# Performance work log

Hardware: AMD Instinct MI355X
Metric: run time of the kernel (lower is better)

Reference implementation:

```python
import jax, jax.numpy as jnp
import numpy as np

SELF_DIM = 6
GS_DIM = 100

def _lin(x, w, b):
    return x @ w + b

def setup_inputs() -> dict:
    key = jax.random.key(0)
    ks = jax.random.split(key, 24)
    def p(k, shape, fan_in):
        return jax.random.normal(k, shape, dtype=jnp.float32) * (1.0 / np.sqrt(fan_in))
    state = jax.random.normal(ks[0], (16384, 20, 13), dtype=jnp.float32)
    inp = {"state": state}
    # mlp1: 13 -> 150 -> 100 -> 100
    inp["w1"], inp["b1"] = p(ks[1], (13, 150), 13), jnp.zeros((150,), jnp.float32)
    inp["w2"], inp["b2"] = p(ks[2], (150, 100), 150), jnp.zeros((100,), jnp.float32)
    inp["w3"], inp["b3"] = p(ks[3], (100, 100), 100), jnp.zeros((100,), jnp.float32)
    # attention: 200 -> 100 -> 100 -> 1
    inp["a1"], inp["ab1"] = p(ks[4], (200, 100), 200), jnp.zeros((100,), jnp.float32)
    inp["a2"], inp["ab2"] = p(ks[5], (100, 100), 100), jnp.zeros((100,), jnp.float32)
    inp["a3"], inp["ab3"] = p(ks[6], (100, 1), 100), jnp.zeros((1,), jnp.float32)
    # mlp2: 106 -> 150 -> 100 -> 100 -> 1
    inp["m1"], inp["mb1"] = p(ks[7], (106, 150), 106), jnp.zeros((150,), jnp.float32)
    inp["m2"], inp["mb2"] = p(ks[8], (150, 100), 150), jnp.zeros((100,), jnp.float32)
    inp["m3"], inp["mb3"] = p(ks[9], (100, 100), 100), jnp.zeros((100,), jnp.float32)
    inp["m4"], inp["mb4"] = p(ks[10], (100, 1), 100), jnp.zeros((1,), jnp.float32)
    return inp

def reference(state, w1, b1, w2, b2, w3, b3, a1, ab1, a2, ab2, a3, ab3,
              m1, mb1, m2, mb2, m3, mb3, m4, mb4):
    B, N, D = state.shape
    self_state = state[:, 0, :SELF_DIM]                      # [B, 6]
    x = state.reshape(B * N, D)
    h = jax.nn.relu(_lin(x, w1, b1))
    h = jax.nn.relu(_lin(h, w2, b2))
    mlp1_out = _lin(h, w3, b3)                               # [B*N, 100]
    feat = mlp1_out.reshape(B, N, GS_DIM)
    global_state = jnp.broadcast_to(feat.mean(axis=1, keepdims=True), (B, N, GS_DIM))
    att_in = jnp.concatenate([feat, global_state], axis=-1)  # [B, N, 200]
    s = jax.nn.relu(_lin(att_in, a1, ab1))
    s = jax.nn.relu(_lin(s, a2, ab2))
    scores = jax.nn.relu(_lin(s, a3, ab3))[..., 0]           # [B, N]
    weights = jax.nn.softmax(scores, axis=1)                 # [B, N]
    weighted_feature = jnp.einsum('bn,bnd->bd', weights, feat)
    joint = jnp.concatenate([self_state, weighted_feature], axis=-1)  # [B, 106]
    v = jax.nn.relu(_lin(joint, m1, mb1))
    v = jax.nn.relu(_lin(v, m2, mb2))
    v = jax.nn.relu(_lin(v, m3, mb3))
    value = _lin(v, m4, mb4)                                 # [B, 1]
    return value
```

## Files before the change

### kernel.cpp

```cpp
#include <hip/hip_runtime.h>
#include <math.h>

#define NTHR 512
#define NB 4
#define NROWSR (NB * 20)

typedef _Float16 h8v __attribute__((ext_vector_type(8)));
typedef _Float16 h2v __attribute__((ext_vector_type(2)));
using f4 = __attribute__((ext_vector_type(4))) float;

__device__ __forceinline__ h2v cvt_pk_h2(float a, float b) {
  return __builtin_bit_cast(h2v, __builtin_amdgcn_cvt_pkrtz(a, b));
}

#define H1_OFF 0
#define H1_PK 168
#define H2_OFF 26880
#define H2_PK 136
#define FEAT_OFF 0
#define FEAT_PK 136
#define S1_OFF 26880
#define S1_PK 136
#define XS_OFF 26880
#define XS_PK 40
#define GS_OFF S1_OFF
#define POOL1 48640

#define L1B 0
#define L2B 20
#define L3B 90
#define A1B 146
#define A2B 202
#define M1B 258
#define M2B 338
#define M3B 408
#define A1GB 464
#define BIAS_BYTE 532480
#define JOINT_BYTE 536576

#define BO_B1 0
#define BO_B2 160
#define BO_B3 320
#define BO_AB1 480
#define BO_MB1 800
#define BO_MB2 960
#define BO_MB3 1120

#define K2ROWS 64
#define K2THR 256
#define K2_JT_OFF 0
#define K2_V1_OFF 17408
#define K2_POOL 38912

__device__ __forceinline__ float relu_f(float v) { return fmaxf(v, 0.f); }
__device__ __forceinline__ float h2f(ushort u) {
  return (float)__builtin_bit_cast(_Float16, u);
}
__device__ __forceinline__ ushort f2h(float v) {
  return __builtin_bit_cast(ushort, (_Float16)v);
}
__device__ __forceinline__ uint pk2h(float a, float b) {
  return (uint)f2h(a) | ((uint)f2h(b) << 16);
}

__device__ __forceinline__ float4 load4_guard(const float* __restrict__ a, int of4, int C) {
  float4 v;
  if (of4 + 3 < C) v = *(const float4*)(a + of4);
  else {
    v.x = (of4 + 0 < C) ? a[of4 + 0] : 0.f;
    v.y = (of4 + 1 < C) ? a[of4 + 1] : 0.f;
    v.z = (of4 + 2 < C) ? a[of4 + 2] : 0.f;
    v.w = (of4 + 3 < C) ? a[of4 + 3] : 0.f;
  }
  return v;
}

__global__ __launch_bounds__(64) void prep_kernel(
    const float* __restrict__ w1, const float* __restrict__ w2,
    const float* __restrict__ w3, const float* __restrict__ a1,
    const float* __restrict__ a2, const float* __restrict__ m1,
    const float* __restrict__ m2, const float* __restrict__ m3,
    const float* __restrict__ b1, const float* __restrict__ b2,
    const float* __restrict__ b3, const float* __restrict__ ab1,
    const float* __restrict__ mb1, const float* __restrict__ mb2,
    const float* __restrict__ mb3,
    uint4* __restrict__ ws) {
  const int job = blockIdx.x;
  const int lane = threadIdx.x;
  if (job == 260) {
    ushort* bh = (ushort*)((char*)ws + BIAS_BYTE);
    for (int idx = lane; idx < 1280; idx += 64) {
      const int reg = idx / 160, off = idx - reg * 160;
      const float* src = nullptr; int C = 0;
      switch (reg) {
        case 0: src = b1;  C = 150; break;
        case 1: src = b2;  C = 100; break;
        case 2: src = b3;  C = 100; break;
        case 3: src = ab1; C = 100; break;
        case 4: src = nullptr; C = 0; break;
        case 5: src = mb1; C = 150; break;
        case 6: src = mb2; C = 100; break;
        default: src = mb3; C = 100; break;
      }
      bh[idx] = (off < C) ? f2h(src[off]) : (ushort)0;
    }
    return;
  }
  const float* W;
  int K, C, NT, base, kb, nt, i;
  if (job < 10)       { W = w1; K = 13;  C = 150; NT = 10; base = L1B; kb = 0; nt = job; }
  else if (job < 45)  { W = w2; K = 150; C = 100; NT = 7;  base = L2B; i = job - 10;  kb = i / 7;  nt = i % 7; }
  else if (job < 73)  { W = w3; K = 100; C = 100; NT = 7;  base = L3B; i = job - 45;  kb = i / 7;  nt = i % 7; }
  else if (job < 101) { W = a1; K = 100; C = 100; NT = 7;  base = A1B; i = job - 73;  kb = i / 7;  nt = i % 7; }
  else if (job < 129) { W = a2; K = 100; C = 100; NT = 7;  base = A2B; i = job - 101; kb = i / 7;  nt = i % 7; }
  else if (job < 169) { W = m1; K = 106; C = 150; NT = 10; base = M1B; i = job - 129; kb = i / 10; nt = i % 10; }
  else if (job < 204) { W = m2; K = 150; C = 100; NT = 7;  base = M2B; i = job - 169; kb = i / 7;  nt = i % 7; }
  else if (job < 232) { W = m3; K = 100; C = 100; NT = 7;  base = M3B; i = job - 204; kb = i / 7;  nt = i % 7; }
  else                { W = a1 + 10000; K = 100; C = 100; NT = 7; base = A1GB; i = job - 232; kb = i / 7; nt = i % 7; }
  const int r = lane & 15, g = lane >> 4;
  const int j = nt * 16 + r;
  uint hi[8], lo[8];
  for (int e = 0; e < 8; ++e) {
    int k = kb * 32 + g * 8 + e;
    float v = (k < K && j < C) ? W[k * C + j] : 0.f;
    _Float16 hh = (_Float16)v;
    float hf = (float)hh;
    _Float16 ll = (_Float16)(v - hf);
    hi[e] = (uint)__builtin_bit_cast(ushort, hh);
    lo[e] = (uint)__builtin_bit_cast(ushort, ll);
  }
  uint4 vh = { hi[0] | (hi[1] << 16), hi[2] | (hi[3] << 16),
               hi[4] | (hi[5] << 16), hi[6] | (hi[7] << 16) };
  uint4 vl = { lo[0] | (lo[1] << 16), lo[2] | (lo[3] << 16),
               lo[4] | (lo[5] << 16), lo[6] | (lo[7] << 16) };
  ws[(size_t)(base + (kb * NT + nt) * 2 + 0) * 64 + lane] = vh;
  ws[(size_t)(base + (kb * NT + nt) * 2 + 1) * 64 + lane] = vl;
}

template <int KB, int NT, int C, int MODE, int ROWS, bool W8, int TERMS>
__device__ __forceinline__ void mfma_layer(
    char* pool, int inOff, int PKin, int outOff, int PKout,
    const h8v* __restrict__ wsB, const ushort* __restrict__ biasH,
    const float* __restrict__ biasF, const ushort* gpartH, float* sceL,
    const float* __restrict__ a3, int lane, int wid) {
  constexpr int MTL = ROWS / 16;
  const int r = lane & 15, g = lane >> 4;
  const char* Ain = pool + inOff;
  int wlo, mtb, mte;
  if constexpr (W8) {
    wlo = wid & 3;
    const int whi = wid >> 2;
    mtb = whi ? 3 : 0; mte = whi ? MTL : 3;
  } else { wlo = wid; mtb = 0; mte = MTL; }
  for (int nt = wlo; nt < NT; nt += 4) {
    h8v wh[KB], wl[KB];
#pragma unroll
    for (int kb = 0; kb < KB; ++kb) {
      wh[kb] = wsB[((kb * NT + nt) * 2 + 0) * 64 + lane];
      if constexpr (TERMS == 2)
        wl[kb] = wsB[((kb * NT + nt) * 2 + 1) * 64 + lane];
    }
    const int of = nt * 16 + g * 4;
    uint2 bp;
    float4 b4, a34;
    if constexpr (MODE == 3) {
      b4 = load4_guard(biasF, of, C);
      a34 = load4_guard(a3, of, C);
    } else {
      bp = *(const uint2*)(biasH + of);
    }
    for (int mt = mtb; mt < mte; ++mt) {
      const int ar = mt * 16 + r;
      f4 acc = {0.f, 0.f, 0.f, 0.f};
      const char* aP = Ain + ar * (PKin * 2) + g * 16;
#pragma unroll
      for (int kb = 0; kb < KB; ++kb) {
        h8v a = *(const h8v*)(aP + kb * 64);
        acc = __builtin_amdgcn_mfma_f32_16x16x32_f16(wh[kb], a, acc, 0, 0, 0);
        if constexpr (TERMS == 2)
          acc = __builtin_amdgcn_mfma_f32_16x16x32_f16(wl[kb], a, acc, 0, 0, 0);
      }
      if constexpr (MODE == 3) {
        float v0 = fmaxf(acc[0] + b4.x, 0.f), v1 = fmaxf(acc[1] + b4.y, 0.f);
        float v2 = fmaxf(acc[2] + b4.z, 0.f), v3 = fmaxf(acc[3] + b4.w, 0.f);
        float val = v0 * a34.x + v1 * a34.y + v2 * a34.z + v3 * a34.w;
        val += __shfl_xor(val, 16);
        val += __shfl_xor(val, 32);
        if (lane < 16) atomicAdd(&sceL[ar], val);
      } else {
        h2v lo = cvt_pk_h2(acc[0], acc[1]);
        h2v hi = cvt_pk_h2(acc[2], acc[3]);
        lo += __builtin_bit_cast(h2v, bp.x);
        hi += __builtin_bit_cast(h2v, bp.y);
        if constexpr (MODE == 2) {
          uint2 gp = *(const uint2*)(gpartH + (ar / 20) * 112 + of);
          lo += __builtin_bit_cast(h2v, gp.x);
          hi += __builtin_bit_cast(h2v, gp.y);
        }
        if constexpr (MODE != 1) {
          h2v z = {(_Float16)0.f, (_Float16)0.f};
          lo = __builtin_elementwise_max(lo, z);
          hi = __builtin_elementwise_max(hi, z);
        }
        *(uint2*)((ushort*)(pool + outOff) + ar * PKout + of) =
            uint2{__builtin_bit_cast(uint, lo), __builtin_bit_cast(uint, hi)};
      }
    }
  }
}

template <int ROWSZ, int PK>
__device__ __forceinline__ void zero_tail(char* pool, int off, int tid) {
  if (tid < ROWSZ) {
    uint4* z = (uint4*)((ushort*)(pool + off) + (size_t)tid * PK + 112);
    z[0] = uint4{0, 0, 0, 0};
    z[1] = uint4{0, 0, 0, 0};
  }
}

__global__ __launch_bounds__(NTHR, 6) void value_net_kernel(
    const float* __restrict__ state,
    const float* __restrict__ ab2,
    const float* __restrict__ a3, const float* __restrict__ ab3,
    const uint4* __restrict__ ws, ushort* __restrict__ jointgH) {
  __shared__ char pool[POOL1];
  __shared__ ushort gpartH[NB * 112];
  __shared__ float sceL[NROWSR], swL[NROWSR];

  const int tid = threadIdx.x;
  const int lane = tid & 63, wid = tid >> 6;
  const int b0 = blockIdx.x * NB;
  const h8v* wsb = (const h8v*)ws;
  const ushort* biasH = (const ushort*)((const char*)ws + BIAS_BYTE);

  for (int i = tid; i < NROWSR * XS_PK; i += NTHR) {
    int row = i / XS_PK, k = i - row * XS_PK;
    float v = (k < 13) ? state[((size_t)b0 * 20 + row) * 13 + k] : 0.f;
    ((ushort*)(pool + XS_OFF))[row * XS_PK + k] = f2h(v);
  }
  if (tid < NROWSR) sceL[tid] = 0.f;
  __syncthreads();

  mfma_layer<1, 10, 150, 0, NROWSR, true, 1>(
      pool, XS_OFF, XS_PK, H1_OFF, H1_PK, wsb + L1B * 64, biasH + BO_B1,
      nullptr, nullptr, nullptr, nullptr, lane, wid);
  __syncthreads();

  zero_tail<NROWSR, H2_PK>(pool, H2_OFF, tid);
  mfma_layer<5, 7, 100, 0, NROWSR, true, 1>(
      pool, H1_OFF, H1_PK, H2_OFF, H2_PK, wsb + L2B * 64, biasH + BO_B2,
      nullptr, nullptr, nullptr, nullptr, lane, wid);
  __syncthreads();

  zero_tail<NROWSR, FEAT_PK>(pool, FEAT_OFF, tid);
  mfma_layer<4, 7, 100, 1, NROWSR, true, 1>(
      pool, H2_OFF, H2_PK, FEAT_OFF, FEAT_PK, wsb + L3B * 64, biasH + BO_B3,
      nullptr, nullptr, nullptr, nullptr, lane, wid);
  __syncthreads();

  if (tid < NB * 100) {
    const int b = tid / 100, d = tid - b * 100;
    const ushort* f = (const ushort*)(pool + FEAT_OFF);
    float s = 0.f;
    for (int n = 0; n < 20; ++n) s += h2f(f[(b * 20 + n) * FEAT_PK + d]);
    ((ushort*)(pool + GS_OFF))[b * 136 + d] = f2h(s * 0.05f);
  } else if (tid < NB * 100 + NB * 28) {
    const int idx = tid - NB * 100;
    ((ushort*)(pool + GS_OFF))[(idx / 28) * 136 + 100 + (idx % 28)] = 0;
  }
  __syncthreads();

  if (wid < 7) {
    const int r = lane & 15, g = lane >> 4;
    const int nt = wid;
    const h8v* wsg = wsb + A1GB * 64;
    h8v wh[4];
#pragma unroll
    for (int kb = 0; kb < 4; ++kb)
      wh[kb] = wsg[((kb * 7 + nt) * 2 + 0) * 64 + lane];
    const char* aP = pool + GS_OFF + (r & 3) * (136 * 2) + g * 16;
    f4 acc = {0.f, 0.f, 0.f, 0.f};
#pragma unroll
    for (int kb = 0; kb < 4; ++kb) {
      h8v a = *(const h8v*)(aP + kb * 64);
      acc = __builtin_amdgcn_mfma_f32_16x16x32_f16(wh[kb], a, acc, 0, 0, 0);
    }
    const int of = nt * 16 + g * 4;
    if (r < 4) {
      uint2 pk = { pk2h(acc[0], acc[1]), pk2h(acc[2], acc[3]) };
      *(uint2*)(gpartH + r * 112 + of) = pk;
    }
  }
  __syncthreads();

  mfma_layer<4, 7, 100, 2, NROWSR, true, 1>(
      pool, FEAT_OFF, FEAT_PK, S1_OFF, S1_PK, wsb + A1B * 64, biasH + BO_AB1,
      nullptr, gpartH, nullptr, nullptr, lane, wid);
  __syncthreads();

  mfma_layer<4, 7, 100, 3, NROWSR, true, 1>(
      pool, S1_OFF, S1_PK, 0, 0, wsb + A2B * 64, nullptr,
      ab2, nullptr, sceL, a3, lane, wid);
  __syncthreads();

  if (tid < 128) {
    const int b = tid >> 5, l = tid & 31;
    const float ab3v = ab3[0];
    float s = (l < 20) ? relu_f(sceL[b * 20 + l] + ab3v) : -1e30f;
    float m = s;
#pragma unroll
    for (int d = 1; d < 32; d <<= 1) m = fmaxf(m, __shfl_xor(m, d));
    float e = (l < 20) ? __expf(s - m) : 0.f;
    float sum = e;
#pragma unroll
    for (int d = 1; d < 32; d <<= 1) sum += __shfl_xor(sum, d);
    if (l < 20) swL[b * 20 + l] = e / sum;
  }
  __syncthreads();

  for (int it = tid; it < NB * 200; it += NTHR) {
    const int b = it / 200, rem = it - b * 200;
    const int d = rem >> 1, half = rem & 1;
    const ushort* f = (const ushort*)(pool + FEAT_OFF);
    float acc = 0.f;
    for (int n = half * 10; n < half * 10 + 10; ++n)
      acc += swL[b * 20 + n] * h2f(f[(b * 20 + n) * FEAT_PK + d]);
    acc += __shfl_xor(acc, 1);
    if (half == 0) jointgH[(size_t)(b0 + b) * 106 + 6 + d] = f2h(acc);
  }
  if (tid < NB * 6) {
    const int b = tid / 6, i = tid - b * 6;
    jointgH[(size_t)(b0 + b) * 106 + i] = f2h(state[((size_t)(b0 + b)) * 260 + i]);
  }
}

__global__ __launch_bounds__(K2THR) void mlp2_kernel(
    const ushort* __restrict__ jointgH,
    const float* __restrict__ m4, const float* __restrict__ mb4,
    const uint4* __restrict__ ws, float* __restrict__ out) {
  __shared__ char pool[K2_POOL];
  __shared__ float m4L[100];
  const int tid = threadIdx.x, lane = tid & 63, wid = tid >> 6;
  const size_t r0 = (size_t)blockIdx.x * K2ROWS;
  const h8v* wsb = (const h8v*)ws;
  const ushort* biasH = (const ushort*)((const char*)ws + BIAS_BYTE);

  for (int i = tid; i < K2ROWS * 136; i += K2THR) {
    int row = i / 136, k = i - row * 136;
    ((ushort*)(pool + K2_JT_OFF))[row * 136 + k] =
        (k < 106) ? jointgH[(r0 + row) * 106 + k] : (ushort)0;
  }
  if (tid < 100) m4L[tid] = m4[tid];
  __syncthreads();

  mfma_layer<4, 10, 150, 0, K2ROWS, false, 2>(
      pool, K2_JT_OFF, 136, K2_V1_OFF, 168, wsb + M1B * 64, biasH + BO_MB1,
      nullptr, nullptr, nullptr, nullptr, lane, wid);
  __syncthreads();

  zero_tail<K2ROWS, 136>(pool, 0, tid);
  mfma_layer<5, 7, 100, 0, K2ROWS, false, 2>(
      pool, K2_V1_OFF, 168, 0, 136, wsb + M2B * 64, biasH + BO_MB2,
      nullptr, nullptr, nullptr, nullptr, lane, wid);
  __syncthreads();

  mfma_layer<4, 7, 100, 0, K2ROWS, false, 2>(
      pool, 0, 136, K2_V1_OFF, 136, wsb + M3B * 64, biasH + BO_MB3,
      nullptr, nullptr, nullptr, nullptr, lane, wid);
  __syncthreads();

  {
    const int row = tid >> 2, seg = tid & 3;
    const ushort* v3 = (const ushort*)(pool + K2_V1_OFF);
    float s = 0.f;
    for (int k = seg; k < 100; k += 4) s += h2f(v3[row * 136 + k]) * m4L[k];
    s += __shfl_xor(s, 1);
    s += __shfl_xor(s, 2);
    if (seg == 0) out[r0 + row] = s + mb4[0];
  }
}

extern "C" void kernel_launch(void* const* d_in, const int* in_sizes, int n_in,
                              void* d_out, int out_size, void* d_ws, size_t ws_size,
                              hipStream_t stream) {
  const float* state = (const float*)d_in[0];
  const float* w1 = (const float*)d_in[1];
  const float* b1 = (const float*)d_in[2];
  const float* w2 = (const float*)d_in[3];
  const float* b2 = (const float*)d_in[4];
  const float* w3 = (const float*)d_in[5];
  const float* b3 = (const float*)d_in[6];
  const float* a1 = (const float*)d_in[7];
  const float* ab1 = (const float*)d_in[8];
  const float* a2 = (const float*)d_in[9];
  const float* ab2 = (const float*)d_in[10];
  const float* a3 = (const float*)d_in[11];
  const float* ab3 = (const float*)d_in[12];
  const float* m1 = (const float*)d_in[13];
  const float* mb1 = (const float*)d_in[14];
  const float* m2 = (const float*)d_in[15];
  const float* mb2 = (const float*)d_in[16];
  const float* m3 = (const float*)d_in[17];
  const float* mb3 = (const float*)d_in[18];
  const float* m4 = (const float*)d_in[19];
  const float* mb4 = (const float*)d_in[20];
  float* out = (float*)d_out;
  uint4* ws = (uint4*)d_ws;
  ushort* jointgH = (ushort*)((char*)d_ws + JOINT_BYTE);

  prep_kernel<<<261, 64, 0, stream>>>(w1, w2, w3, a1, a2, m1, m2, m3,
                                      b1, b2, b3, ab1, mb1, mb2, mb3, ws);

  const int B = in_sizes[0] / 260;
  value_net_kernel<<<dim3(B / NB), dim3(NTHR), 0, stream>>>(
      state, ab2, a3, ab3, (const uint4*)ws, jointgH);

  mlp2_kernel<<<dim3(B / K2ROWS), dim3(K2THR), 0, stream>>>(
      jointgH, m4, mb4, (const uint4*)ws, out);
}
```

Baseline: 123.8 us.

## Pair adjacent N-tiles per wave in MLP1/attention layers and fuse softmax with pooling

In the first kernel, each wave now processes two adjacent 16-column output tiles per iteration, reusing each loaded A fragment for two MFMAs. This halves the A-operand LDS reads per output column and gives the MFMA pipe two independent accumulator chains, at the cost of more live weight registers. The softmax and weighted-feature pooling are merged into one per-batch wave that broadcasts weights by shuffle, removing the swL buffer and one block barrier. Work now runs across only four waves instead of all threads.

```diff
diff --git a/kernel.cpp b/kernel.cpp
--- a/kernel.cpp
+++ b/kernel.cpp
@@ -137,7 +137,7 @@
   ws[(size_t)(base + (kb * NT + nt) * 2 + 1) * 64 + lane] = vl;
 }
 
-template <int KB, int NT, int C, int MODE, int ROWS, bool W8, int TERMS>
+template <int KB, int NT, int C, int MODE, int ROWS, bool W8, int TERMS, bool PAIR>
 __device__ __forceinline__ void mfma_layer(
     char* pool, int inOff, int PKin, int outOff, int PKout,
     const h8v* __restrict__ wsB, const ushort* __restrict__ biasH,
@@ -152,58 +152,142 @@
     const int whi = wid >> 2;
     mtb = whi ? 3 : 0; mte = whi ? MTL : 3;
   } else { wlo = wid; mtb = 0; mte = MTL; }
-  for (int nt = wlo; nt < NT; nt += 4) {
-    h8v wh[KB], wl[KB];
-#pragma unroll
-    for (int kb = 0; kb < KB; ++kb) {
-      wh[kb] = wsB[((kb * NT + nt) * 2 + 0) * 64 + lane];
-      if constexpr (TERMS == 2)
-        wl[kb] = wsB[((kb * NT + nt) * 2 + 1) * 64 + lane];
+
+  if constexpr (PAIR) {
+    constexpr int NP2 = (NT + 1) / 2;
+    for (int p = wlo; p < NP2; p += 4) {
+      const int nt0 = 2 * p;
+      const bool two = (nt0 + 1 < NT);
+      h8v w0[KB], w1[KB];
+#pragma unroll
+      for (int kb = 0; kb < KB; ++kb) {
+        w0[kb] = wsB[((kb * NT + nt0) * 2 + 0) * 64 + lane];
+        if (two) w1[kb] = wsB[((kb * NT + nt0 + 1) * 2 + 0) * 64 + lane];
+      }
+      const int of0 = nt0 * 16 + g * 4, of1 = of0 + 16;
+      uint2 bp0, bp1;
+      float4 b40, b41, a340, a341;
+      if constexpr (MODE == 3) {
+        b40 = load4_guard(biasF, of0, C); a340 = load4_guard(a3, of0, C);
+        b41 = load4_guard(biasF, of1, C); a341 = load4_guard(a3, of1, C);
+      } else {
+        bp0 = *(const uint2*)(biasH + of0);
+        bp1 = *(const uint2*)(biasH + of1);
+      }
+      for (int mt = mtb; mt < mte; ++mt) {
+        const int ar = mt * 16 + r;
+        f4 acc0 = {0.f, 0.f, 0.f, 0.f}, acc1 = {0.f, 0.f, 0.f, 0.f};
+        const char* aP = Ain + ar * (PKin * 2) + g * 16;
+#pragma unroll
+        for (int kb = 0; kb < KB; ++kb) {
+          h8v a = *(const h8v*)(aP + kb * 64);
+          acc0 = __builtin_amdgcn_mfma_f32_16x16x32_f16(w0[kb], a, acc0, 0, 0, 0);
+          if (two) acc1 = __builtin_amdgcn_mfma_f32_16x16x32_f16(w1[kb], a, acc1, 0, 0, 0);
+        }
+        if constexpr (MODE == 3) {
+          float v0 = fmaxf(acc0[0] + b40.x, 0.f), v1 = fmaxf(acc0[1] + b40.y, 0.f);
+          float v2 = fmaxf(acc0[2] + b40.z, 0.f), v3 = fmaxf(acc0[3] + b40.w, 0.f);
+          float val = v0 * a340.x + v1 * a340.y + v2 * a340.z + v3 * a340.w;
+          if (two) {
+            float u0 = fmaxf(acc1[0] + b41.x, 0.f), u1 = fmaxf(acc1[1] + b41.y, 0.f);
+            float u2 = fmaxf(acc1[2] + b41.z, 0.f), u3 = fmaxf(acc1[3] + b41.w, 0.f);
+            val += u0 * a341.x + u1 * a341.y + u2 * a341.z + u3 * a341.w;
+          }
+          val += __shfl_xor(val, 16);
+          val += __shfl_xor(val, 32);
+          if (lane < 16) atomicAdd(&sceL[ar], val);
+        } else {
+          h2v lo = cvt_pk_h2(acc0[0], acc0[1]);
+          h2v hi = cvt_pk_h2(acc0[2], acc0[3]);
+          lo += __builtin_bit_cast(h2v, bp0.x);
+          hi += __builtin_bit_cast(h2v, bp0.y);
+          if constexpr (MODE == 2) {
+            uint2 gp = *(const uint2*)(gpartH + (ar / 20) * 112 + of0);
+            lo += __builtin_bit_cast(h2v, gp.x);
+            hi += __builtin_bit_cast(h2v, gp.y);
+          }
+          if constexpr (MODE != 1) {
+            h2v z = {(_Float16)0.f, (_Float16)0.f};
+            lo = __builtin_elementwise_max(lo, z);
+            hi = __builtin_elementwise_max(hi, z);
+          }
+          *(uint2*)((ushort*)(pool + outOff) + ar * PKout + of0) =
+              uint2{__builtin_bit_cast(uint, lo), __builtin_bit_cast(uint, hi)};
+          if (two) {
+            h2v lo1 = cvt_pk_h2(acc1[0], acc1[1]);
+            h2v hi1 = cvt_pk_h2(acc1[2], acc1[3]);
+            lo1 += __builtin_bit_cast(h2v, bp1.x);
+            hi1 += __builtin_bit_cast(h2v, bp1.y);
+            if constexpr (MODE == 2) {
+              uint2 gp1 = *(const uint2*)(gpartH + (ar / 20) * 112 + of1);
+              lo1 += __builtin_bit_cast(h2v, gp1.x);
+              hi1 += __builtin_bit_cast(h2v, gp1.y);
+            }
+            if constexpr (MODE != 1) {
+              h2v z = {(_Float16)0.f, (_Float16)0.f};
+              lo1 = __builtin_elementwise_max(lo1, z);
+              hi1 = __builtin_elementwise_max(hi1, z);
+            }
+            *(uint2*)((ushort*)(pool + outOff) + ar * PKout + of1) =
+                uint2{__builtin_bit_cast(uint, lo1), __builtin_bit_cast(uint, hi1)};
+          }
+        }
+      }
     }
-    const int of = nt * 16 + g * 4;
-    uint2 bp;
-    float4 b4, a34;
-    if constexpr (MODE == 3) {
-      b4 = load4_guard(biasF, of, C);
-      a34 = load4_guard(a3, of, C);
-    } else {
-      bp = *(const uint2*)(biasH + of);
-    }
-    for (int mt = mtb; mt < mte; ++mt) {
-      const int ar = mt * 16 + r;
-      f4 acc = {0.f, 0.f, 0.f, 0.f};
-      const char* aP = Ain + ar * (PKin * 2) + g * 16;
+  } else {
+    for (int nt = wlo; nt < NT; nt += 4) {
+      h8v wh[KB], wl[KB];
 #pragma unroll
       for (int kb = 0; kb < KB; ++kb) {
-        h8v a = *(const h8v*)(aP + kb * 64);
-        acc = __builtin_amdgcn_mfma_f32_16x16x32_f16(wh[kb], a, acc, 0, 0, 0);
+        wh[kb] = wsB[((kb * NT + nt) * 2 + 0) * 64 + lane];
         if constexpr (TERMS == 2)
-          acc = __builtin_amdgcn_mfma_f32_16x16x32_f16(wl[kb], a, acc, 0, 0, 0);
-      }
+          wl[kb] = wsB[((kb * NT + nt) * 2 + 1) * 64 + lane];
+      }
+      const int of = nt * 16 + g * 4;
+      uint2 bp;
+      float4 b4, a34;
       if constexpr (MODE == 3) {
-        float v0 = fmaxf(acc[0] + b4.x, 0.f), v1 = fmaxf(acc[1] + b4.y, 0.f);
-        float v2 = fmaxf(acc[2] + b4.z, 0.f), v3 = fmaxf(acc[3] + b4.w, 0.f);
-        float val = v0 * a34.x + v1 * a34.y + v2 * a34.z + v3 * a34.w;
-        val += __shfl_xor(val, 16);
-        val += __shfl_xor(val, 32);
-        if (lane < 16) atomicAdd(&sceL[ar], val);
+        b4 = load4_guard(biasF, of, C);
+        a34 = load4_guard(a3, of, C);
       } else {
-        h2v lo = cvt_pk_h2(acc[0], acc[1]);
-        h2v hi = cvt_pk_h2(acc[2], acc[3]);
-        lo += __builtin_bit_cast(h2v, bp.x);
-        hi += __builtin_bit_cast(h2v, bp.y);
-        if constexpr (MODE == 2) {
-          uint2 gp = *(const uint2*)(gpartH + (ar / 20) * 112 + of);
-          lo += __builtin_bit_cast(h2v, gp.x);
-          hi += __builtin_bit_cast(h2v, gp.y);
+        bp = *(const uint2*)(biasH + of);
+      }
+      for (int mt = mtb; mt < mte; ++mt) {
+        const int ar = mt * 16 + r;
+        f4 acc = {0.f, 0.f, 0.f, 0.f};
+        const char* aP = Ain + ar * (PKin * 2) + g * 16;
+#pragma unroll
+        for (int kb = 0; kb < KB; ++kb) {
+          h8v a = *(const h8v*)(aP + kb * 64);
+          acc = __builtin_amdgcn_mfma_f32_16x16x32_f16(wh[kb], a, acc, 0, 0, 0);
+          if constexpr (TERMS == 2)
+            acc = __builtin_amdgcn_mfma_f32_16x16x32_f16(wl[kb], a, acc, 0, 0, 0);
         }
-        if constexpr (MODE != 1) {
-          h2v z = {(_Float16)0.f, (_Float16)0.f};
-          lo = __builtin_elementwise_max(lo, z);
-          hi = __builtin_elementwise_max(hi, z);
+        if constexpr (MODE == 3) {
+          float v0 = fmaxf(acc[0] + b4.x, 0.f), v1 = fmaxf(acc[1] + b4.y, 0.f);
+          float v2 = fmaxf(acc[2] + b4.z, 0.f), v3 = fmaxf(acc[3] + b4.w, 0.f);
+          float val = v0 * a34.x + v1 * a34.y + v2 * a34.z + v3 * a34.w;
+          val += __shfl_xor(val, 16);
+          val += __shfl_xor(val, 32);
+          if (lane < 16) atomicAdd(&sceL[ar], val);
+        } else {
+          h2v lo = cvt_pk_h2(acc[0], acc[1]);
+          h2v hi = cvt_pk_h2(acc[2], acc[3]);
+          lo += __builtin_bit_cast(h2v, bp.x);
+          hi += __builtin_bit_cast(h2v, bp.y);
+          if constexpr (MODE == 2) {
+            uint2 gp = *(const uint2*)(gpartH + (ar / 20) * 112 + of);
+            lo += __builtin_bit_cast(h2v, gp.x);
+            hi += __builtin_bit_cast(h2v, gp.y);
+          }
+          if constexpr (MODE != 1) {
+            h2v z = {(_Float16)0.f, (_Float16)0.f};
+            lo = __builtin_elementwise_max(lo, z);
+            hi = __builtin_elementwise_max(hi, z);
+          }
+          *(uint2*)((ushort*)(pool + outOff) + ar * PKout + of) =
+              uint2{__builtin_bit_cast(uint, lo), __builtin_bit_cast(uint, hi)};
         }
-        *(uint2*)((ushort*)(pool + outOff) + ar * PKout + of) =
-            uint2{__builtin_bit_cast(uint, lo), __builtin_bit_cast(uint, hi)};
       }
     }
   }
@@ -225,7 +309,7 @@
     const uint4* __restrict__ ws, ushort* __restrict__ jointgH) {
   __shared__ char pool[POOL1];
   __shared__ ushort gpartH[NB * 112];
-  __shared__ float sceL[NROWSR], swL[NROWSR];
+  __shared__ float sceL[NROWSR];
 
   const int tid = threadIdx.x;
   const int lane = tid & 63, wid = tid >> 6;
@@ -241,19 +325,19 @@
   if (tid < NROWSR) sceL[tid] = 0.f;
   __syncthreads();
 
-  mfma_layer<1, 10, 150, 0, NROWSR, true, 1>(
+  mfma_layer<1, 10, 150, 0, NROWSR, true, 1, true>(
       pool, XS_OFF, XS_PK, H1_OFF, H1_PK, wsb + L1B * 64, biasH + BO_B1,
       nullptr, nullptr, nullptr, nullptr, lane, wid);
   __syncthreads();
 
   zero_tail<NROWSR, H2_PK>(pool, H2_OFF, tid);
-  mfma_layer<5, 7, 100, 0, NROWSR, true, 1>(
+  mfma_layer<5, 7, 100, 0, NROWSR, true, 1, true>(
       pool, H1_OFF, H1_PK, H2_OFF, H2_PK, wsb + L2B * 64, biasH + BO_B2,
       nullptr, nullptr, nullptr, nullptr, lane, wid);
   __syncthreads();
 
   zero_tail<NROWSR, FEAT_PK>(pool, FEAT_OFF, tid);
-  mfma_layer<4, 7, 100, 1, NROWSR, true, 1>(
+  mfma_layer<4, 7, 100, 1, NROWSR, true, 1, true>(
       pool, H2_OFF, H2_PK, FEAT_OFF, FEAT_PK, wsb + L3B * 64, biasH + BO_B3,
       nullptr, nullptr, nullptr, nullptr, lane, wid);
   __syncthreads();
@@ -293,44 +377,41 @@
   }
   __syncthreads();
 
-  mfma_layer<4, 7, 100, 2, NROWSR, true, 1>(
+  mfma_layer<4, 7, 100, 2, NROWSR, true, 1, true>(
       pool, FEAT_OFF, FEAT_PK, S1_OFF, S1_PK, wsb + A1B * 64, biasH + BO_AB1,
       nullptr, gpartH, nullptr, nullptr, lane, wid);
   __syncthreads();
 
-  mfma_layer<4, 7, 100, 3, NROWSR, true, 1>(
+  mfma_layer<4, 7, 100, 3, NROWSR, true, 1, true>(
       pool, S1_OFF, S1_PK, 0, 0, wsb + A2B * 64, nullptr,
       ab2, nullptr, sceL, a3, lane, wid);
   __syncthreads();
 
-  if (tid < 128) {
-    const int b = tid >> 5, l = tid & 31;
+  if (wid < NB) {
+    const int b = wid;
     const float ab3v = ab3[0];
-    float s = (l < 20) ? relu_f(sceL[b * 20 + l] + ab3v) : -1e30f;
+    float s = (lane < 20) ? relu_f(sceL[b * 20 + lane] + ab3v) : -1e30f;
     float m = s;
 #pragma unroll
-    for (int d = 1; d < 32; d <<= 1) m = fmaxf(m, __shfl_xor(m, d));
-    float e = (l < 20) ? __expf(s - m) : 0.f;
+    for (int d = 1; d < 64; d <<= 1) m = fmaxf(m, __shfl_xor(m, d));
+    float e = (lane < 20) ? __expf(s - m) : 0.f;
     float sum = e;
 #pragma unroll
-    for (int d = 1; d < 32; d <<= 1) sum += __shfl_xor(sum, d);
-    if (l < 20) swL[b * 20 + l] = e / sum;
-  }
-  __syncthreads();
-
-  for (int it = tid; it < NB * 200; it += NTHR) {
-    const int b = it / 200, rem = it - b * 200;
-    const int d = rem >> 1, half = rem & 1;
+    for (int d = 1; d < 64; d <<= 1) sum += __shfl_xor(sum, d);
+    const float rinv = 1.f / sum;
     const ushort* f = (const ushort*)(pool + FEAT_OFF);
-    float acc = 0.f;
-    for (int n = half * 10; n < half * 10 + 10; ++n)
-      acc += swL[b * 20 + n] * h2f(f[(b * 20 + n) * FEAT_PK + d]);
-    acc += __shfl_xor(acc, 1);
-    if (half == 0) jointgH[(size_t)(b0 + b) * 106 + 6 + d] = f2h(acc);
-  }
-  if (tid < NB * 6) {
-    const int b = tid / 6, i = tid - b * 6;
-    jointgH[(size_t)(b0 + b) * 106 + i] = f2h(state[((size_t)(b0 + b)) * 260 + i]);
+    const int d0 = lane, d1 = lane + 64;
+    float acc0 = 0.f, acc1 = 0.f;
+    for (int n = 0; n < 20; ++n) {
+      const float swn = __shfl(e, n) * rinv;
+      const ushort* frow = f + (b * 20 + n) * FEAT_PK;
+      acc0 += swn * h2f(frow[d0]);
+      if (d1 < 100) acc1 += swn * h2f(frow[d1]);
+    }
+    ushort* jb = jointgH + (size_t)(b0 + b) * 106;
+    if (d0 < 100) jb[6 + d0] = f2h(acc0);
+    if (d1 < 100) jb[6 + d1] = f2h(acc1);
+    if (lane < 6) jb[lane] = f2h(state[((size_t)(b0 + b)) * 260 + lane]);
   }
 }
 
@@ -353,18 +434,18 @@
   if (tid < 100) m4L[tid] = m4[tid];
   __syncthreads();
 
-  mfma_layer<4, 10, 150, 0, K2ROWS, false, 2>(
+  mfma_layer<4, 10, 150, 0, K2ROWS, false, 2, false>(
       pool, K2_JT_OFF, 136, K2_V1_OFF, 168, wsb + M1B * 64, biasH + BO_MB1,
       nullptr, nullptr, nullptr, nullptr, lane, wid);
   __syncthreads();
 
   zero_tail<K2ROWS, 136>(pool, 0, tid);
-  mfma_layer<5, 7, 100, 0, K2ROWS, false, 2>(
+  mfma_layer<5, 7, 100, 0, K2ROWS, false, 2, false>(
       pool, K2_V1_OFF, 168, 0, 136, wsb + M2B * 64, biasH + BO_MB2,
       nullptr, nullptr, nullptr, nullptr, lane, wid);
   __syncthreads();
 
-  mfma_layer<4, 7, 100, 0, K2ROWS, false, 2>(
+  mfma_layer<4, 7, 100, 0, K2ROWS, false, 2, false>(
       pool, 0, 136, K2_V1_OFF, 136, wsb + M3B * 64, biasH + BO_MB3,
       nullptr, nullptr, nullptr, nullptr, lane, wid);
   __syncthreads();
```

After: 126.1 us. No clear change (+1.9%).
